# Performance work log

Measured on AMD Instinct MI355X. Metric: run time of the kernel, lower is better.

Reference implementation:

```python
import jax, jax.numpy as jnp
import numpy as np
from jax import lax

RADIUS = 2
DILATION = 2
KS = 2 * RADIUS + 1  # 5
PERM = np.array([6, 8, 1, 11, 2, 10, 0, 7, 9, 4, 5, 3])


def _shift_kernels():
    # Reproduce the torch index construction in numpy (all constants).
    six = np.array([[0, 1, 1], [1, 1, 0], [1, 0, 1], [1, 1, 2], [2, 1, 1], [1, 2, 1]])
    # pairwise squared distances between the 6 neighbourhood offsets
    d = ((six[:, None, :] - six[None, :, :]) ** 2).sum(-1)
    x, y = np.meshgrid(np.arange(6), np.arange(6), indexing='ij')
    mask = (x > y).reshape(-1) & (d == 2).reshape(-1)
    idx1 = np.repeat(six[:, None, :], 6, axis=1).reshape(-1, 3)[mask]
    idx2 = np.repeat(six[None, :, :], 6, axis=0).reshape(-1, 3)[mask]
    k1 = np.zeros((12, 1, 3, 3, 3), np.float32)
    k2 = np.zeros((12, 1, 3, 3, 3), np.float32)
    r = np.arange(12)
    k1[r, 0, idx1[:, 0], idx1[:, 1], idx1[:, 2]] = 1.0
    k2[r, 0, idx2[:, 0], idx2[:, 1], idx2[:, 2]] = 1.0
    return jnp.asarray(k1), jnp.asarray(k2)

_K1, _K2 = _shift_kernels()
DN = ('NCDHW', 'OIDHW', 'NCDHW')


def _rep_pad(x, p):
    return jnp.pad(x, ((0, 0), (0, 0), (p, p), (p, p), (p, p)), mode='edge')


def mindssc(img):
    # img: [N,1,D,H,W]
    p1 = _rep_pad(img, DILATION)
    c1 = lax.conv_general_dilated(p1, _K1, (1, 1, 1), 'VALID',
                                  rhs_dilation=(DILATION,) * 3, dimension_numbers=DN)
    c2 = lax.conv_general_dilated(p1, _K2, (1, 1, 1), 'VALID',
                                  rhs_dilation=(DILATION,) * 3, dimension_numbers=DN)
    diff2 = (c1 - c2) ** 2  # [N,12,D,H,W]
    p2 = _rep_pad(diff2, RADIUS)
    ssd = lax.reduce_window(p2, 0.0, lax.add, (1, 1, KS, KS, KS),
                            (1, 1, 1, 1, 1), 'VALID') / float(KS ** 3)
    mind = ssd - jnp.min(ssd, axis=1, keepdims=True)
    mind_var = jnp.mean(mind, axis=1, keepdims=True)
    m = jnp.mean(mind_var)
    mind_var = jnp.clip(mind_var, m * 0.001, m * 1000.0)
    mind = jnp.exp(-mind / mind_var)
    return mind[:, PERM]


def setup_inputs() -> dict:
    key = jax.random.key(0)
    k1, k2 = jax.random.split(key)
    shape = (1, 1, 128, 128, 128)
    return {
        'y_true': jax.random.normal(k1, shape, dtype=jnp.float32),
        'y_pred': jax.random.normal(k2, shape, dtype=jnp.float32),
    }


def reference(y_true, y_pred):
    return jnp.mean((mindssc(y_pred) - mindssc(y_true)) ** 2)
```

## Files before the change

### kernel.cpp

```cpp
#include <hip/hip_runtime.h>

#define DIM   128
#define DMASK 127
#define PLANE (DIM * DIM)
#define VOX   (1 << 21)
#define NCH   12

#define CHS   (VOX + 2048)
#define IMGS  (NCH * CHS + 1024)

typedef __attribute__((ext_vector_type(2))) _Float16 half2v;
typedef __attribute__((ext_vector_type(4))) _Float16 half4v;

#define D2S 136
#define T1S 128

__constant__ int c_sd1[12] = { 0, 0, 0, 0, 0, 2, 2, 2, 0, 0, 0, 0};
__constant__ int c_sh1[12] = { 0,-2,-2, 0, 0, 0, 0, 0, 2, 2, 2, 2};
__constant__ int c_sw1[12] = {-2, 0, 0, 2, 2, 0, 0, 0, 0, 0, 0, 0};
__constant__ int c_sd2[12] = {-2,-2, 0,-2, 0, 0, 0, 0,-2, 0, 0, 2};
__constant__ int c_sh2[12] = { 0, 0, 0, 0,-2, 0,-2, 0, 0, 0, 0, 0};
__constant__ int c_sw2[12] = { 0, 0,-2, 0, 0,-2, 0, 2, 0,-2, 2, 0};

__device__ __forceinline__ int clamp7(int v) { return min(max(v, 0), DMASK); }

__global__ __launch_bounds__(256) void f123(const float* __restrict__ img0,
                                            const float* __restrict__ img1,
                                            _Float16* __restrict__ Sall) {
    const float* img = blockIdx.y ? img1 : img0;
    _Float16* outS = Sall + (size_t)blockIdx.y * IMGS;

    int b  = blockIdx.x;
    int ch = b >> 5;
    int hq = (b >> 3) & 3;
    int ds = b & 7;
    int h0 = hq << 5;
    int d0 = ds << 4;
    int tid = threadIdx.x;

    __shared__ int rowA[36], rowB[36];
    __shared__ __align__(16) _Float16 D2p[36 * D2S];
    __shared__ __align__(16) float    T1[36 * T1S];

    int sd1 = c_sd1[ch], sh1 = c_sh1[ch], sw1 = c_sw1[ch];
    int sd2 = c_sd2[ch], sh2 = c_sh2[ch], sw2 = c_sw2[ch];

    if (tid < 36) {
        int hqr = clamp7(h0 - 2 + tid);
        rowA[tid] = clamp7(hqr + sh1) * (DIM * 4);
        rowB[tid] = clamp7(hqr + sh2) * (DIM * 4);
    }
    __syncthreads();

    int l  = tid & 63;
    int rr = tid >> 6;
    int wp  = (tid & 63) << 1;
    int lh0 = (tid >> 6) << 3;

    int cAi = 0, cBi = 0;
    if (l < 62) {
        int j0 = 4 + (l << 1);
        cAi = (j0 - 2 + sw1) * 4;
        cBi = (j0 - 2 + sw2) * 4;
    }

    float2 win[8];
    half2v hist[5][8];
#pragma unroll
    for (int k = 0; k < 8; ++k) {
        win[k].x = 0.0f; win[k].y = 0.0f;
#pragma unroll
        for (int s = 0; s < 5; ++s) hist[s][k] = half2v{(_Float16)0.0f, (_Float16)0.0f};
    }

    _Float16* dstBase = outS + (size_t)ch * CHS + (h0 + lh0) * DIM + wp;

    for (int oo = 0; oo < 4; ++oo) {
#pragma unroll
        for (int s = 0; s < 5; ++s) {
            int it = oo * 5 + s;
            int dp = clamp7(d0 - 2 + it);
            const char* pA = (const char*)(img + clamp7(dp + sd1) * PLANE);
            const char* pB = (const char*)(img + clamp7(dp + sd2) * PLANE);

            if (l < 62) {
                int j0 = 4 + (l << 1);
#pragma unroll
                for (int k = 0; k < 9; ++k) {
                    int r = rr + (k << 2);
                    float2 a = *(const float2*)(pA + rowA[r] + cAi);
                    float2 c = *(const float2*)(pB + rowB[r] + cBi);
                    float e0 = a.x - c.x, e1 = a.y - c.y;
                    half2v hv = { (_Float16)(e0 * e0), (_Float16)(e1 * e1) };
                    *(half2v*)&D2p[r * D2S + j0] = hv;
                }
            }
            if (tid < 144) {
                int r  = tid >> 2;
                int pe = tid & 3;
                int j0 = (pe < 2) ? (pe << 1) : (124 + (pe << 1));
                int ra = rowA[r], rb = rowB[r];
                float dd[2];
#pragma unroll
                for (int e = 0; e < 2; ++e) {
                    int wq = clamp7(j0 + e - 2);
                    float a = *(const float*)(pA + ra + clamp7(wq + sw1) * 4);
                    float c = *(const float*)(pB + rb + clamp7(wq + sw2) * 4);
                    float df = a - c;
                    dd[e] = df * df;
                }
                half2v hv = { (_Float16)dd[0], (_Float16)dd[1] };
                *(half2v*)&D2p[r * D2S + j0] = hv;
            }
            __syncthreads();

            for (int i = tid; i < 36 * 32; i += 256) {
                int r = i >> 5;
                int g = (i & 31) << 2;
                const half4v* src = (const half4v*)&D2p[r * D2S + g];
                half4v lo = src[0], hi = src[1];
                float l0 = lo[0], l1 = lo[1], l2 = lo[2], l3 = lo[3];
                float u0 = hi[0], u1 = hi[1], u2 = hi[2], u3 = hi[3];
                float o0 = l0 + l1 + l2 + l3 + u0;
                float o1 = o0 - l0 + u1;
                float o2 = o1 - l1 + u2;
                float o3 = o2 - l2 + u3;
                *(float4*)&T1[r * T1S + g] = make_float4(o0, o1, o2, o3);
            }
            __syncthreads();

            {
                const float* base = &T1[lh0 * T1S + wp];
                float rx[12], ry[12];
#pragma unroll
                for (int k = 0; k < 12; ++k) {
                    float2 v = *(const float2*)(base + k * T1S);
                    rx[k] = v.x; ry[k] = v.y;
                }
                float sx = rx[0] + rx[1] + rx[2] + rx[3] + rx[4];
                float sy = ry[0] + ry[1] + ry[2] + ry[3] + ry[4];
                bool dowrite = (it >= 4);
                _Float16* dstD = dstBase + (size_t)(d0 + it - 4) * PLANE;
#pragma unroll
                for (int k = 0; k < 8; ++k) {
                    half2v hv = { (_Float16)sx, (_Float16)sy };
                    half2v old = hist[s][k];
                    win[k].x += (float)hv[0] - (float)old[0];
                    win[k].y += (float)hv[1] - (float)old[1];
                    hist[s][k] = hv;
                    if (dowrite) {
                        half2v ov = { (_Float16)win[k].x, (_Float16)win[k].y };
                        *(half2v*)(dstD + k * DIM) = ov;
                    }
                    if (k < 7) {
                        sx += rx[k + 5] - rx[k];
                        sy += ry[k + 5] - ry[k];
                    }
                }
            }
        }
    }
}

__global__ __launch_bounds__(256, 3) void kmse(const _Float16* __restrict__ S0,
                                               const _Float16* __restrict__ S1,
                                               float* __restrict__ partial) {
    int t = blockIdx.x * 256 + threadIdx.x;

    half4v v0[NCH], v1[NCH];
#pragma unroll
    for (int ch = 0; ch < NCH; ++ch)
        v0[ch] = ((const half4v*)(S0 + (size_t)ch * CHS))[t];
#pragma unroll
    for (int ch = 0; ch < NCH; ++ch)
        v1[ch] = ((const half4v*)(S1 + (size_t)ch * CHS))[t];

    float mn0[4], sm0[4], mn1[4], sm1[4];
#pragma unroll
    for (int j = 0; j < 4; ++j) {
        mn0[j] = 3.4e38f; sm0[j] = 0.0f;
        mn1[j] = 3.4e38f; sm1[j] = 0.0f;
    }
#pragma unroll
    for (int ch = 0; ch < NCH; ++ch)
#pragma unroll
        for (int j = 0; j < 4; ++j) {
            float s0 = (float)v0[ch][j];
            float s1 = (float)v1[ch][j];
            mn0[j] = fminf(mn0[j], s0); sm0[j] += s0;
            mn1[j] = fminf(mn1[j], s1); sm1[j] += s1;
        }

    float inv0[4], inv1[4];
#pragma unroll
    for (int j = 0; j < 4; ++j) {
        inv0[j] = __fdividef(1.0f, sm0[j] * (1.0f / 12.0f) - mn0[j]);
        inv1[j] = __fdividef(1.0f, sm1[j] * (1.0f / 12.0f) - mn1[j]);
    }

    float acc = 0.0f;
#pragma unroll
    for (int ch = 0; ch < NCH; ++ch)
#pragma unroll
        for (int j = 0; j < 4; ++j) {
            float e0 = __expf(-((float)v0[ch][j] - mn0[j]) * inv0[j]);
            float e1 = __expf(-((float)v1[ch][j] - mn1[j]) * inv1[j]);
            float df = e0 - e1;
            acc += df * df;
        }

#pragma unroll
    for (int off = 32; off > 0; off >>= 1)
        acc += __shfl_down(acc, off, 64);
    __shared__ float smem[4];
    int lane = threadIdx.x & 63, wv = threadIdx.x >> 6;
    if (lane == 0) smem[wv] = acc;
    __syncthreads();
    if (threadIdx.x == 0)
        partial[blockIdx.x] = smem[0] + smem[1] + smem[2] + smem[3];
}

__global__ __launch_bounds__(256) void kred(const float* __restrict__ partial,
                                            float* __restrict__ out) {
    int tid = threadIdx.x;
    float acc = 0.0f;
#pragma unroll
    for (int k = 0; k < 8; ++k)
        acc += partial[tid + (k << 8)];
#pragma unroll
    for (int off = 32; off > 0; off >>= 1)
        acc += __shfl_down(acc, off, 64);
    __shared__ float smem[4];
    int lane = tid & 63, wv = tid >> 6;
    if (lane == 0) smem[wv] = acc;
    __syncthreads();
    if (tid == 0)
        out[0] = (smem[0] + smem[1] + smem[2] + smem[3])
               * (1.0f / (12.0f * (float)VOX));
}

__global__ void kdiag(float* out, float ws_mb) { out[0] = ws_mb; }

extern "C" void kernel_launch(void* const* d_in, const int* in_sizes, int n_in,
                              void* d_out, int out_size, void* d_ws, size_t ws_size,
                              hipStream_t stream) {
    const float* y_true = (const float*)d_in[0];
    const float* y_pred = (const float*)d_in[1];
    float* out = (float*)d_out;

    const size_t NEED = 2ull * IMGS * sizeof(_Float16) + 8192 + 64;
    if (ws_size < NEED) {
        kdiag<<<1, 1, 0, stream>>>(out, (float)(ws_size >> 20));
        return;
    }

    _Float16* S0      = (_Float16*)d_ws;
    _Float16* S1      = S0 + (size_t)IMGS;
    float*    partial = (float*)(S1 + (size_t)IMGS);

    f123<<<dim3(12 * 4 * 8, 2), 256, 0, stream>>>(y_true, y_pred, S0);
    kmse<<<VOX / 4 / 256, 256, 0, stream>>>(S0, S1, partial);
    kred<<<1, 256, 0, stream>>>(partial, out);
}
```

Before: 142.2 us.

## Fuse W-axis box filter into difference load and double-buffer fp16 shared tile

Each thread now loads the six clamped neighbouring voxels it needs directly from global memory and computes the W-direction 5-tap sum in registers. This removes the separate squared-difference shared buffer, one pass over shared memory and one barrier per depth slice. The intermediate tile is stored as fp16 in a double-buffered array, so the next slice's write does not need a barrier against the previous slice's read. In exchange each thread issues about three times as many scalar global loads (overlapping, mostly cache hits), and the W-sums are rounded to half precision.

```diff
diff --git a/kernel.cpp b/kernel.cpp
--- a/kernel.cpp
+++ b/kernel.cpp
@@ -11,9 +11,6 @@
 
 typedef __attribute__((ext_vector_type(2))) _Float16 half2v;
 typedef __attribute__((ext_vector_type(4))) _Float16 half4v;
-
-#define D2S 136
-#define T1S 128
 
 __constant__ int c_sd1[12] = { 0, 0, 0, 0, 0, 2, 2, 2, 0, 0, 0, 0};
 __constant__ int c_sh1[12] = { 0,-2,-2, 0, 0, 0, 0, 0, 2, 2, 2, 2};
@@ -39,8 +36,7 @@
     int tid = threadIdx.x;
 
     __shared__ int rowA[36], rowB[36];
-    __shared__ __align__(16) _Float16 D2p[36 * D2S];
-    __shared__ __align__(16) float    T1[36 * T1S];
+    __shared__ __align__(16) _Float16 T1[2][36 * 128];
 
     int sd1 = c_sd1[ch], sh1 = c_sh1[ch], sw1 = c_sw1[ch];
     int sd2 = c_sd2[ch], sh2 = c_sh2[ch], sw2 = c_sw2[ch];
@@ -50,18 +46,18 @@
         rowA[tid] = clamp7(hqr + sh1) * (DIM * 4);
         rowB[tid] = clamp7(hqr + sh2) * (DIM * 4);
     }
-    __syncthreads();
 
     int l  = tid & 63;
-    int rr = tid >> 6;
-    int wp  = (tid & 63) << 1;
-    int lh0 = (tid >> 6) << 3;
-
-    int cAi = 0, cBi = 0;
-    if (l < 62) {
-        int j0 = 4 + (l << 1);
-        cAi = (j0 - 2 + sw1) * 4;
-        cBi = (j0 - 2 + sw2) * 4;
+    int rq = tid >> 6;
+    int wp  = l << 1;
+    int lh0 = rq << 3;
+
+    int offA[6], offB[6];
+#pragma unroll
+    for (int e = 0; e < 6; ++e) {
+        int wb = clamp7((l << 1) - 2 + e);
+        offA[e] = clamp7(wb + sw1) * 4;
+        offB[e] = clamp7(wb + sw2) * 4;
     }
 
     float2 win[8];
@@ -74,6 +70,8 @@
     }
 
     _Float16* dstBase = outS + (size_t)ch * CHS + (h0 + lh0) * DIM + wp;
+
+    __syncthreads();
 
     for (int oo = 0; oo < 4; ++oo) {
 #pragma unroll
@@ -82,60 +80,35 @@
             int dp = clamp7(d0 - 2 + it);
             const char* pA = (const char*)(img + clamp7(dp + sd1) * PLANE);
             const char* pB = (const char*)(img + clamp7(dp + sd2) * PLANE);
-
-            if (l < 62) {
-                int j0 = 4 + (l << 1);
-#pragma unroll
-                for (int k = 0; k < 9; ++k) {
-                    int r = rr + (k << 2);
-                    float2 a = *(const float2*)(pA + rowA[r] + cAi);
-                    float2 c = *(const float2*)(pB + rowB[r] + cBi);
-                    float e0 = a.x - c.x, e1 = a.y - c.y;
-                    half2v hv = { (_Float16)(e0 * e0), (_Float16)(e1 * e1) };
-                    *(half2v*)&D2p[r * D2S + j0] = hv;
-                }
-            }
-            if (tid < 144) {
-                int r  = tid >> 2;
-                int pe = tid & 3;
-                int j0 = (pe < 2) ? (pe << 1) : (124 + (pe << 1));
-                int ra = rowA[r], rb = rowB[r];
-                float dd[2];
-#pragma unroll
-                for (int e = 0; e < 2; ++e) {
-                    int wq = clamp7(j0 + e - 2);
-                    float a = *(const float*)(pA + ra + clamp7(wq + sw1) * 4);
-                    float c = *(const float*)(pB + rb + clamp7(wq + sw2) * 4);
+            _Float16* Tc = T1[it & 1];
+
+#pragma unroll
+            for (int k = 0; k < 9; ++k) {
+                int r = rq + (k << 2);
+                const char* ra = pA + rowA[r];
+                const char* rb = pB + rowB[r];
+                float dd[6];
+#pragma unroll
+                for (int e = 0; e < 6; ++e) {
+                    float a = *(const float*)(ra + offA[e]);
+                    float c = *(const float*)(rb + offB[e]);
                     float df = a - c;
                     dd[e] = df * df;
                 }
-                half2v hv = { (_Float16)dd[0], (_Float16)dd[1] };
-                *(half2v*)&D2p[r * D2S + j0] = hv;
+                float o0 = dd[0] + dd[1] + dd[2] + dd[3] + dd[4];
+                float o1 = o0 - dd[0] + dd[5];
+                half2v hv = { (_Float16)o0, (_Float16)o1 };
+                *(half2v*)&Tc[r * 128 + (l << 1)] = hv;
             }
             __syncthreads();
 
-            for (int i = tid; i < 36 * 32; i += 256) {
-                int r = i >> 5;
-                int g = (i & 31) << 2;
-                const half4v* src = (const half4v*)&D2p[r * D2S + g];
-                half4v lo = src[0], hi = src[1];
-                float l0 = lo[0], l1 = lo[1], l2 = lo[2], l3 = lo[3];
-                float u0 = hi[0], u1 = hi[1], u2 = hi[2], u3 = hi[3];
-                float o0 = l0 + l1 + l2 + l3 + u0;
-                float o1 = o0 - l0 + u1;
-                float o2 = o1 - l1 + u2;
-                float o3 = o2 - l2 + u3;
-                *(float4*)&T1[r * T1S + g] = make_float4(o0, o1, o2, o3);
-            }
-            __syncthreads();
-
             {
-                const float* base = &T1[lh0 * T1S + wp];
+                const _Float16* base = &Tc[lh0 * 128 + wp];
                 float rx[12], ry[12];
 #pragma unroll
                 for (int k = 0; k < 12; ++k) {
-                    float2 v = *(const float2*)(base + k * T1S);
-                    rx[k] = v.x; ry[k] = v.y;
+                    half2v v = *(const half2v*)(base + k * 128);
+                    rx[k] = (float)v[0]; ry[k] = (float)v[1];
                 }
                 float sx = rx[0] + rx[1] + rx[2] + rx[3] + rx[4];
                 float sy = ry[0] + ry[1] + ry[2] + ry[3] + ry[4];
```

Measured after the change: 267.7 us. 1.88x slower.
